# Kernel tuning notes

Hardware: AMD Instinct MI355X
Metric: run time of the kernel (lower is better)

The kernel has to match this reference:

```python
import jax, jax.numpy as jnp
import numpy as np

# dims
B, S, D, H, F = 4, 1024, 1024, 16, 4096
DH = D // H
THETA0 = 1.0   # base firing threshold of AdaptiveLIFNeuron
RHO = 0.9      # adaptation decay
EPS = 1e-5


def layer_norm(x, g, b):
    mu = jnp.mean(x, axis=-1, keepdims=True)
    var = jnp.mean((x - mu) ** 2, axis=-1, keepdims=True)
    return (x - mu) * jax.lax.rsqrt(var + EPS) * g + b


def spike(u):
    # Heaviside forward, sigmoid surrogate gradient (straight-through)
    sg = jax.nn.sigmoid(4.0 * u)
    hard = (u > 0).astype(u.dtype)
    return sg + jax.lax.stop_gradient(hard - sg)


def setup_inputs() -> dict:
    key = jax.random.key(0)
    ks = jax.random.split(key, 8)
    std = 0.02
    w = lambda k, shape: jax.random.normal(k, shape, jnp.float32) * std
    return {
        "x": jax.random.normal(ks[0], (B, S, D), jnp.float32),
        "Wq": w(ks[1], (D, D)), "bq": jnp.zeros((D,), jnp.float32),
        "Wk": w(ks[2], (D, D)), "bk": jnp.zeros((D,), jnp.float32),
        "Wv": w(ks[3], (D, D)), "bv": jnp.zeros((D,), jnp.float32),
        "Wo": w(ks[4], (D, D)), "bo": jnp.zeros((D,), jnp.float32),
        "g1": jnp.ones((D,), jnp.float32), "b1": jnp.zeros((D,), jnp.float32),
        "W1": w(ks[5], (D, F)), "bf1": jnp.zeros((F,), jnp.float32),
        "W2": w(ks[6], (F, D)), "bf2": jnp.zeros((D,), jnp.float32),
        "g2": jnp.ones((D,), jnp.float32), "b2": jnp.zeros((D,), jnp.float32),
        "decay": jnp.full((F,), 0.8, jnp.float32),  # per-feature membrane leak
        "beta": jnp.full((F,), 0.1, jnp.float32),   # per-feature threshold adaptation
    }


def reference(x, Wq, bq, Wk, bk, Wv, bv, Wo, bo, g1, b1, W1, bf1, W2, bf2, g2, b2, decay, beta):
    # --- causal multi-head self-attention (DSALayer) ---
    q = (x @ Wq + bq).reshape(B, S, H, DH)
    k = (x @ Wk + bk).reshape(B, S, H, DH)
    v = (x @ Wv + bv).reshape(B, S, H, DH)
    scores = jnp.einsum("bqhd,bkhd->bhqk", q, k) / np.sqrt(DH).astype(np.float32)
    causal = jnp.tril(jnp.ones((S, S), bool))
    scores = jnp.where(causal, scores, jnp.asarray(-1e9, scores.dtype))
    p = jax.nn.softmax(scores, axis=-1)
    attn = jnp.einsum("bhqk,bkhd->bqhd", p, v).reshape(B, S, D) @ Wo + bo
    h = layer_norm(x + attn, g1, b1)

    # --- feed-forward with per-timestep adaptive LIF recurrence ---
    ff = h @ W1 + bf1                      # [B, S, F]

    def step(carry, xt):
        vm, a = carry                      # membrane potential, adaptation
        vm = decay * vm + xt
        u = vm - (THETA0 + a)
        s = spike(u)
        vm = vm * (1.0 - s)                # hard reset on spike
        a = RHO * a + beta * s
        return (vm, a), s

    init = (jnp.zeros((B, F), x.dtype), jnp.zeros((B, F), x.dtype))
    _, spikes = jax.lax.scan(step, init, jnp.swapaxes(ff, 0, 1))  # scan over time
    spikes = jnp.swapaxes(spikes, 0, 1)    # [B, S, F]

    ff_out = spikes @ W2 + bf2
    return layer_norm(h + ff_out, g2, b2)
```

## Files before the change

### kernel.cpp

```cpp
#include <hip/hip_runtime.h>
#include <hip/hip_bf16.h>
#include <stdint.h>

#define Bsz 4
#define Ssz 1024
#define Dsz 1024
#define Hsz 16
#define Fsz 4096

typedef __hip_bfloat16 bf16;
typedef __attribute__((ext_vector_type(8))) short bf16x8;
typedef __attribute__((ext_vector_type(4))) float f32x4;

typedef __attribute__((address_space(1))) const void gvoid_t;
typedef __attribute__((address_space(3))) void svoid_t;

__device__ __forceinline__ void gload16(const bf16* g, bf16* l) {
    __builtin_amdgcn_global_load_lds((gvoid_t*)g, (svoid_t*)l, 16, 0, 0);
}

__global__ __launch_bounds__(256) void split_k(const float* __restrict__ src,
                                               bf16* __restrict__ hi,
                                               bf16* __restrict__ lo,
                                               const float* __restrict__ bq,
                                               const float* __restrict__ bk,
                                               const float* __restrict__ bv,
                                               float* __restrict__ bqkv) {
    const int i = (blockIdx.x * 256 + threadIdx.x) * 4;
    const float4 v = *(const float4*)(src + i);
    float vv[4] = {v.x, v.y, v.z, v.w};
    #pragma unroll
    for (int u = 0; u < 4; ++u) {
        const bf16 h = __float2bfloat16(vv[u]);
        hi[i + u] = h;
        lo[i + u] = __float2bfloat16(vv[u] - __bfloat162float(h));
    }
    if (blockIdx.x < 3) {
        const float* bsrc = (blockIdx.x == 0) ? bq : (blockIdx.x == 1) ? bk : bv;
        const int j = threadIdx.x * 4;
        *(float4*)(bqkv + blockIdx.x * 1024 + j) = *(const float4*)(bsrc + j);
    }
}

__global__ __launch_bounds__(256) void transpose_split4_k(const float* __restrict__ Wq,
                                                          const float* __restrict__ Wk,
                                                          const float* __restrict__ Wv,
                                                          const float* __restrict__ Wo,
                                                          bf16* __restrict__ qkv_hi,
                                                          bf16* __restrict__ qkv_lo,
                                                          bf16* __restrict__ wo_hi,
                                                          bf16* __restrict__ wo_lo) {
    __shared__ float tile[32][33];
    const int z = blockIdx.z;
    const float* in = (z == 0) ? Wq : (z == 1) ? Wk : (z == 2) ? Wv : Wo;
    const size_t WP = (size_t)Dsz * Dsz;
    bf16* hiT = (z < 3) ? qkv_hi + (size_t)z * WP : wo_hi;
    bf16* loT = (z < 3) ? qkv_lo + (size_t)z * WP : wo_lo;
    const int bx = blockIdx.x * 32, by = blockIdx.y * 32;
    const int tx = threadIdx.x, ty = threadIdx.y;
    #pragma unroll
    for (int i = 0; i < 32; i += 8)
        tile[ty + i][tx] = in[(size_t)(by + ty + i) * Dsz + bx + tx];
    __syncthreads();
    #pragma unroll
    for (int i = 0; i < 32; i += 8) {
        const float v = tile[tx][ty + i];
        const bf16 h = __float2bfloat16(v);
        const size_t o = (size_t)(bx + ty + i) * Dsz + by + tx;
        hiT[o] = h;
        loT[o] = __float2bfloat16(v - __bfloat162float(h));
    }
}

__global__ __launch_bounds__(256) void transpose_split_k(const float* __restrict__ in,
                                                         bf16* __restrict__ hiT,
                                                         bf16* __restrict__ loT,
                                                         int R, int C) {
    __shared__ float tile[32][33];
    const int bx = blockIdx.x * 32, by = blockIdx.y * 32;
    const int tx = threadIdx.x, ty = threadIdx.y;
    #pragma unroll
    for (int i = 0; i < 32; i += 8)
        tile[ty + i][tx] = in[(size_t)(by + ty + i) * C + bx + tx];
    __syncthreads();
    #pragma unroll
    for (int i = 0; i < 32; i += 8) {
        const float v = tile[tx][ty + i];
        const bf16 h = __float2bfloat16(v);
        const size_t o = (size_t)(bx + ty + i) * R + by + tx;
        hiT[o] = h;
        loT[o] = __float2bfloat16(v - __bfloat162float(h));
    }
}

__global__ __launch_bounds__(256) void transpose_cast_k(const float* __restrict__ in,
                                                        bf16* __restrict__ outT,
                                                        int R, int C) {
    __shared__ float tile[32][33];
    const int bx = blockIdx.x * 32, by = blockIdx.y * 32;
    const int tx = threadIdx.x, ty = threadIdx.y;
    #pragma unroll
    for (int i = 0; i < 32; i += 8)
        tile[ty + i][tx] = in[(size_t)(by + ty + i) * C + bx + tx];
    __syncthreads();
    #pragma unroll
    for (int i = 0; i < 32; i += 8)
        outT[(size_t)(bx + ty + i) * R + by + tx] = __float2bfloat16(tile[tx][ty + i]);
}

__global__ __launch_bounds__(256) void gemm3_bt(const bf16* __restrict__ Ah,
                                                const bf16* __restrict__ Al,
                                                const bf16* __restrict__ Bh,
                                                const bf16* __restrict__ Bl,
                                                const float* __restrict__ bias,
                                                float* __restrict__ Cf,
                                                int M, int N, int K) {
    __shared__ alignas(16) bf16 Ash[128 * 32];
    __shared__ alignas(16) bf16 Asl[128 * 32];
    __shared__ alignas(16) bf16 Bsh[128 * 32];
    __shared__ alignas(16) bf16 Bsl[128 * 32];
    const int t = threadIdx.x;
    const int lane = t & 63, wv = t >> 6;
    const int mw = wv >> 1, nw = wv & 1;
    const int m0 = blockIdx.y * 128, n0 = blockIdx.x * 128;
    const int z = blockIdx.z, nz = gridDim.z;
    const int Ks = K / nz, koff = z * Ks;
    const int r16 = lane & 15, q8 = (lane >> 4) * 8;
    const int arow = t >> 2, acol = (t & 3) * 8;

    const bf16* gAh = Ah + (size_t)(m0 + arow) * K + koff + acol;
    const bf16* gAl = Al + (size_t)(m0 + arow) * K + koff + acol;
    const bf16* gBh = Bh + (size_t)(n0 + arow) * K + koff + acol;
    const bf16* gBl = Bl + (size_t)(n0 + arow) * K + koff + acol;
    const size_t rK64 = (size_t)64 * K;
    bf16* lAh = Ash + wv * 512;
    bf16* lAl = Asl + wv * 512;
    bf16* lBh = Bsh + wv * 512;
    bf16* lBl = Bsl + wv * 512;

    f32x4 acc[4][4] = {};

    for (int k0 = 0; k0 < Ks; k0 += 32) {
        __syncthreads();
        gload16(gAh + k0, lAh);  gload16(gAh + k0 + rK64, lAh + 2048);
        gload16(gAl + k0, lAl);  gload16(gAl + k0 + rK64, lAl + 2048);
        gload16(gBh + k0, lBh);  gload16(gBh + k0 + rK64, lBh + 2048);
        gload16(gBl + k0, lBl);  gload16(gBl + k0 + rK64, lBl + 2048);
        __syncthreads();

        bf16x8 ah[4], al[4], bh[4], bl[4];
        #pragma unroll
        for (int rt = 0; rt < 4; ++rt) {
            const int ro = (64 * mw + 16 * rt + r16) * 32 + q8;
            ah[rt] = *(const bf16x8*)(Ash + ro);
            al[rt] = *(const bf16x8*)(Asl + ro);
        }
        #pragma unroll
        for (int ct = 0; ct < 4; ++ct) {
            const int co = (64 * nw + 16 * ct + r16) * 32 + q8;
            bh[ct] = *(const bf16x8*)(Bsh + co);
            bl[ct] = *(const bf16x8*)(Bsl + co);
        }
        #pragma unroll
        for (int rt = 0; rt < 4; ++rt)
            #pragma unroll
            for (int ct = 0; ct < 4; ++ct) {
                acc[rt][ct] = __builtin_amdgcn_mfma_f32_16x16x32_bf16(ah[rt], bh[ct], acc[rt][ct], 0, 0, 0);
                acc[rt][ct] = __builtin_amdgcn_mfma_f32_16x16x32_bf16(ah[rt], bl[ct], acc[rt][ct], 0, 0, 0);
                acc[rt][ct] = __builtin_amdgcn_mfma_f32_16x16x32_bf16(al[rt], bh[ct], acc[rt][ct], 0, 0, 0);
            }
    }

    float* Cz = Cf + (size_t)z * M * N;
    const int rowi = (lane >> 4) * 4;
    const int coli = lane & 15;
    #pragma unroll
    for (int ct = 0; ct < 4; ++ct) {
        const int col = n0 + 64 * nw + 16 * ct + coli;
        const float bv = (z == 0) ? bias[col] : 0.f;
        #pragma unroll
        for (int rt = 0; rt < 4; ++rt) {
            const int rowb = m0 + 64 * mw + 16 * rt + rowi;
            #pragma unroll
            for (int r = 0; r < 4; ++r)
                Cz[(size_t)(rowb + r) * N + col] = acc[rt][ct][r] + bv;
        }
    }
}

__global__ __launch_bounds__(256) void gemm3_qkv(const bf16* __restrict__ Ah,
                                                 const bf16* __restrict__ Al,
                                                 const bf16* __restrict__ Bh,
                                                 const bf16* __restrict__ Bl,
                                                 const float* __restrict__ bias,
                                                 bf16* __restrict__ qhi, bf16* __restrict__ qlo,
                                                 bf16* __restrict__ khi, bf16* __restrict__ klo,
                                                 bf16* __restrict__ vthi, bf16* __restrict__ vtlo) {
    const int K = Dsz;
    __shared__ alignas(16) bf16 Ash[128 * 32];
    __shared__ alignas(16) bf16 Asl[128 * 32];
    __shared__ alignas(16) bf16 Bsh[128 * 32];
    __shared__ alignas(16) bf16 Bsl[128 * 32];
    const int t = threadIdx.x;
    const int lane = t & 63, wv = t >> 6;
    const int mw = wv >> 1, nw = wv & 1;
    const int m0 = blockIdx.y * 128, n0 = blockIdx.x * 128;
    const int r16 = lane & 15, q8 = (lane >> 4) * 8;
    const int arow = t >> 2, acol = (t & 3) * 8;

    const bf16* gAh = Ah + (size_t)(m0 + arow) * K + acol;
    const bf16* gAl = Al + (size_t)(m0 + arow) * K + acol;
    const bf16* gBh = Bh + (size_t)(n0 + arow) * K + acol;
    const bf16* gBl = Bl + (size_t)(n0 + arow) * K + acol;
    const size_t rK64 = (size_t)64 * K;
    bf16* lAh = Ash + wv * 512;
    bf16* lAl = Asl + wv * 512;
    bf16* lBh = Bsh + wv * 512;
    bf16* lBl = Bsl + wv * 512;

    f32x4 acc[4][4] = {};

    for (int k0 = 0; k0 < K; k0 += 32) {
        __syncthreads();
        gload16(gAh + k0, lAh);  gload16(gAh + k0 + rK64, lAh + 2048);
        gload16(gAl + k0, lAl);  gload16(gAl + k0 + rK64, lAl + 2048);
        gload16(gBh + k0, lBh);  gload16(gBh + k0 + rK64, lBh + 2048);
        gload16(gBl + k0, lBl);  gload16(gBl + k0 + rK64, lBl + 2048);
        __syncthreads();

        bf16x8 ah[4], al[4], bh[4], bl[4];
        #pragma unroll
        for (int rt = 0; rt < 4; ++rt) {
            const int ro = (64 * mw + 16 * rt + r16) * 32 + q8;
            ah[rt] = *(const bf16x8*)(Ash + ro);
            al[rt] = *(const bf16x8*)(Asl + ro);
        }
        #pragma unroll
        for (int ct = 0; ct < 4; ++ct) {
            const int co = (64 * nw + 16 * ct + r16) * 32 + q8;
            bh[ct] = *(const bf16x8*)(Bsh + co);
            bl[ct] = *(const bf16x8*)(Bsl + co);
        }
        #pragma unroll
        for (int rt = 0; rt < 4; ++rt)
            #pragma unroll
            for (int ct = 0; ct < 4; ++ct) {
                acc[rt][ct] = __builtin_amdgcn_mfma_f32_16x16x32_bf16(ah[rt], bh[ct], acc[rt][ct], 0, 0, 0);
                acc[rt][ct] = __builtin_amdgcn_mfma_f32_16x16x32_bf16(ah[rt], bl[ct], acc[rt][ct], 0, 0, 0);
                acc[rt][ct] = __builtin_amdgcn_mfma_f32_16x16x32_bf16(al[rt], bh[ct], acc[rt][ct], 0, 0, 0);
            }
    }

    const int rowi = (lane >> 4) * 4;
    const int coli = lane & 15;
    if (n0 < 2048) {
        const float scale = (n0 < 1024) ? 0.125f : 1.0f;
        bf16* hip_ = (n0 < 1024) ? qhi : khi;
        bf16* lop_ = (n0 < 1024) ? qlo : klo;
        const int cbase = (n0 < 1024) ? n0 : (n0 - 1024);
        #pragma unroll
        for (int ct = 0; ct < 4; ++ct) {
            const int col = cbase + 64 * nw + 16 * ct + coli;
            const float bv = bias[n0 + 64 * nw + 16 * ct + coli];
            #pragma unroll
            for (int rt = 0; rt < 4; ++rt) {
                const int rowb = m0 + 64 * mw + 16 * rt + rowi;
                #pragma unroll
                for (int r = 0; r < 4; ++r) {
                    const float val = (acc[rt][ct][r] + bv) * scale;
                    const bf16 h = __float2bfloat16(val);
                    const size_t off = (size_t)(rowb + r) * Dsz + col;
                    hip_[off] = h;
                    lop_[off] = __float2bfloat16(val - __bfloat162float(h));
                }
            }
        }
    } else {
        #pragma unroll
        for (int ct = 0; ct < 4; ++ct) {
            const int col = n0 + 64 * nw + 16 * ct + coli;
            const float bv = bias[col];
            const int c2 = col - 2048;
            #pragma unroll
            for (int rt = 0; rt < 4; ++rt) {
                const int rowb = m0 + 64 * mw + 16 * rt + rowi;
                const int b = rowb >> 10, s = rowb & 1023;
                bf16 hv[4], lv[4];
                #pragma unroll
                for (int r = 0; r < 4; ++r) {
                    const float val = acc[rt][ct][r] + bv;
                    hv[r] = __float2bfloat16(val);
                    lv[r] = __float2bfloat16(val - __bfloat162float(hv[r]));
                }
                const size_t vo = (size_t)b * (16 * 64 * 1024) + (size_t)c2 * 1024 + s;
                *(uint2*)&vthi[vo] = *(const uint2*)hv;
                *(uint2*)&vtlo[vo] = *(const uint2*)lv;
            }
        }
    }
}

__global__ __launch_bounds__(256) void gemm1_bt(const bf16* __restrict__ A,
                                                const bf16* __restrict__ Bt,
                                                const float* __restrict__ bias,
                                                float* __restrict__ Cf,
                                                int M, int N, int K) {
    __shared__ alignas(16) bf16 As[128 * 32];
    __shared__ alignas(16) bf16 Bs[128 * 32];
    const int t = threadIdx.x;
    const int lane = t & 63, wv = t >> 6;
    const int mw = wv >> 1, nw = wv & 1;
    const int m0 = blockIdx.y * 128, n0 = blockIdx.x * 128;
    const int z = blockIdx.z, nz = gridDim.z;
    const int Ks = K / nz, koff = z * Ks;
    const int r16 = lane & 15, q8 = (lane >> 4) * 8;
    const int arow = t >> 2, acol = (t & 3) * 8;

    const bf16* gA = A + (size_t)(m0 + arow) * K + koff + acol;
    const bf16* gB = Bt + (size_t)(n0 + arow) * K + koff + acol;
    const size_t rK64 = (size_t)64 * K;
    bf16* lA = As + wv * 512;
    bf16* lB = Bs + wv * 512;

    f32x4 acc[4][4] = {};

    for (int k0 = 0; k0 < Ks; k0 += 32) {
        __syncthreads();
        gload16(gA + k0, lA);  gload16(gA + k0 + rK64, lA + 2048);
        gload16(gB + k0, lB);  gload16(gB + k0 + rK64, lB + 2048);
        __syncthreads();

        bf16x8 af[4], bf_[4];
        #pragma unroll
        for (int rt = 0; rt < 4; ++rt)
            af[rt] = *(const bf16x8*)(As + (64 * mw + 16 * rt + r16) * 32 + q8);
        #pragma unroll
        for (int ct = 0; ct < 4; ++ct)
            bf_[ct] = *(const bf16x8*)(Bs + (64 * nw + 16 * ct + r16) * 32 + q8);
        #pragma unroll
        for (int rt = 0; rt < 4; ++rt)
            #pragma unroll
            for (int ct = 0; ct < 4; ++ct)
                acc[rt][ct] = __builtin_amdgcn_mfma_f32_16x16x32_bf16(
                    af[rt], bf_[ct], acc[rt][ct], 0, 0, 0);
    }

    float* Cz = Cf + (size_t)z * M * N;
    const int rowi = (lane >> 4) * 4;
    const int coli = lane & 15;
    #pragma unroll
    for (int ct = 0; ct < 4; ++ct) {
        const int col = n0 + 64 * nw + 16 * ct + coli;
        const float bv = (z == 0) ? bias[col] : 0.f;
        #pragma unroll
        for (int rt = 0; rt < 4; ++rt) {
            const int rowb = m0 + 64 * mw + 16 * rt + rowi;
            #pragma unroll
            for (int r = 0; r < 4; ++r)
                Cz[(size_t)(rowb + r) * N + col] = acc[rt][ct][r] + bv;
        }
    }
}

__global__ __launch_bounds__(512) void attn_mfma_k(const bf16* __restrict__ qhp,
                                                   const bf16* __restrict__ qlp,
                                                   const bf16* __restrict__ khp,
                                                   const bf16* __restrict__ klp,
                                                   const bf16* __restrict__ vhp,
                                                   const bf16* __restrict__ vlp,
                                                   bf16* __restrict__ ohi,
                                                   bf16* __restrict__ olo) {
    __shared__ alignas(16) float Pf[256 * 68];

    const int bh = blockIdx.x;
    const int b = bh >> 4, h = bh & 15;
    const int pr = blockIdx.y;
    const int t = threadIdx.x, w = t >> 6, lane = t & 63;
    const int r16 = lane & 15, quad = lane >> 4;
    const int strip = (w < 4) ? pr : 7 - pr;
    const int qw = strip * 128 + 32 * (w & 3);

    bf16x8 aQh[2][2], aQl[2][2];
    #pragma unroll
    for (int mt = 0; mt < 2; ++mt) {
        const size_t qb = (size_t)(b * Ssz + qw + 16 * mt + r16) * Dsz + h * 64 + quad * 8;
        aQh[mt][0] = *(const bf16x8*)(qhp + qb);
        aQh[mt][1] = *(const bf16x8*)(qhp + qb + 32);
        aQl[mt][0] = *(const bf16x8*)(qlp + qb);
        aQl[mt][1] = *(const bf16x8*)(qlp + qb + 32);
    }

    f32x4 aco[2][4] = {};
    float lrun[2][4] = {};
    const int ntiles = (qw + 31) / 64 + 1;

    for (int kt = 0; kt < ntiles; ++kt) {
        #pragma unroll
        for (int nt = 0; nt < 4; ++nt) {
            const size_t kb = (size_t)(b * Ssz + kt * 64 + nt * 16 + r16) * Dsz + h * 64 + quad * 8;
            const bf16x8 bKh0 = *(const bf16x8*)(khp + kb);
            const bf16x8 bKh1 = *(const bf16x8*)(khp + kb + 32);
            const bf16x8 bKl0 = *(const bf16x8*)(klp + kb);
            const bf16x8 bKl1 = *(const bf16x8*)(klp + kb + 32);
            const int key = kt * 64 + nt * 16 + r16;
            #pragma unroll
            for (int mt = 0; mt < 2; ++mt) {
                f32x4 s = {};
                s = __builtin_amdgcn_mfma_f32_16x16x32_bf16(aQh[mt][0], bKh0, s, 0, 0, 0);
                s = __builtin_amdgcn_mfma_f32_16x16x32_bf16(aQh[mt][0], bKl0, s, 0, 0, 0);
                s = __builtin_amdgcn_mfma_f32_16x16x32_bf16(aQl[mt][0], bKh0, s, 0, 0, 0);
                s = __builtin_amdgcn_mfma_f32_16x16x32_bf16(aQh[mt][1], bKh1, s, 0, 0, 0);
                s = __builtin_amdgcn_mfma_f32_16x16x32_bf16(aQh[mt][1], bKl1, s, 0, 0, 0);
                s = __builtin_amdgcn_mfma_f32_16x16x32_bf16(aQl[mt][1], bKh1, s, 0, 0, 0);
                #pragma unroll
                for (int r = 0; r < 4; ++r) {
                    const int qrow = qw + 16 * mt + quad * 4 + r;
                    const float p = (key <= qrow) ? __expf(s[r]) : 0.f;
                    lrun[mt][r] += p;
                    Pf[(32 * w + 16 * mt + quad * 4 + r) * 68 + nt * 16 + r16] = p;
                }
            }
        }

        bf16x8 aPh[2][2], aPl[2][2];
        #pragma unroll
        for (int mt = 0; mt < 2; ++mt)
            #pragma unroll
            for (int ks = 0; ks < 2; ++ks) {
                const float* pr_ = &Pf[(32 * w + 16 * mt + r16) * 68 + ks * 32 + quad * 8];
                const float4 pa = *(const float4*)pr_;
                const float4 pb = *(const float4*)(pr_ + 4);
                const float pv[8] = {pa.x, pa.y, pa.z, pa.w, pb.x, pb.y, pb.z, pb.w};
                bf16 hv[8], lv[8];
                #pragma unroll
                for (int j = 0; j < 8; ++j) {
                    hv[j] = __float2bfloat16(pv[j]);
                    lv[j] = __float2bfloat16(pv[j] - __bfloat162float(hv[j]));
                }
                aPh[mt][ks] = *(const bf16x8*)hv;
                aPl[mt][ks] = *(const bf16x8*)lv;
            }

        #pragma unroll
        for (int nt = 0; nt < 4; ++nt) {
            const size_t vb = ((size_t)bh * 64 + nt * 16 + r16) * Ssz + kt * 64 + quad * 8;
            const bf16x8 bVh0 = *(const bf16x8*)(vhp + vb);
            const bf16x8 bVh1 = *(const bf16x8*)(vhp + vb + 32);
            const bf16x8 bVl0 = *(const bf16x8*)(vlp + vb);
            const bf16x8 bVl1 = *(const bf16x8*)(vlp + vb + 32);
            #pragma unroll
            for (int mt = 0; mt < 2; ++mt) {
                aco[mt][nt] = __builtin_amdgcn_mfma_f32_16x16x32_bf16(aPh[mt][0], bVh0, aco[mt][nt], 0, 0, 0);
                aco[mt][nt] = __builtin_amdgcn_mfma_f32_16x16x32_bf16(aPh[mt][0], bVl0, aco[mt][nt], 0, 0, 0);
                aco[mt][nt] = __builtin_amdgcn_mfma_f32_16x16x32_bf16(aPl[mt][0], bVh0, aco[mt][nt], 0, 0, 0);
                aco[mt][nt] = __builtin_amdgcn_mfma_f32_16x16x32_bf16(aPh[mt][1], bVh1, aco[mt][nt], 0, 0, 0);
                aco[mt][nt] = __builtin_amdgcn_mfma_f32_16x16x32_bf16(aPh[mt][1], bVl1, aco[mt][nt], 0, 0, 0);
                aco[mt][nt] = __builtin_amdgcn_mfma_f32_16x16x32_bf16(aPl[mt][1], bVh1, aco[mt][nt], 0, 0, 0);
            }
        }
    }

    #pragma unroll
    for (int mt = 0; mt < 2; ++mt)
        #pragma unroll
        for (int r = 0; r < 4; ++r) {
            float l = lrun[mt][r];
            l += __shfl_xor(l, 1); l += __shfl_xor(l, 2);
            l += __shfl_xor(l, 4); l += __shfl_xor(l, 8);
            lrun[mt][r] = l;
        }
    #pragma unroll
    for (int mt = 0; mt < 2; ++mt)
        #pragma unroll
        for (int nt = 0; nt < 4; ++nt)
            #pragma unroll
            for (int r = 0; r < 4; ++r) {
                const size_t off = (size_t)(b * Ssz + qw + 16 * mt + quad * 4 + r) * Dsz
                                   + h * 64 + nt * 16 + r16;
                const float val = aco[mt][nt][r] / lrun[mt][r];
                const bf16 hh = __float2bfloat16(val);
                ohi[off] = hh;
                olo[off] = __float2bfloat16(val - __bfloat162float(hh));
            }
}

__global__ __launch_bounds__(64) void scan_k(const float* __restrict__ ff,
                                             const float* __restrict__ decay,
                                             const float* __restrict__ beta,
                                             bf16* __restrict__ spikes) {
    const int idx = blockIdx.x * 64 + threadIdx.x;
    const int b = idx >> 12;
    const int f = idx & (Fsz - 1);
    const float dec = decay[f];
    const float bet = beta[f];
    const float* src = ff + (size_t)b * Ssz * Fsz + f;
    bf16* dst = spikes + (size_t)b * Ssz * Fsz + f;
    float vm = 0.f, a = 0.f;
    float buf[64];
    #pragma unroll
    for (int u = 0; u < 64; ++u) buf[u] = src[(size_t)u * Fsz];
    for (int gg = 0; gg < 16; ++gg) {
        #pragma unroll
        for (int sub = 0; sub < 4; ++sub) {
            const int g = gg * 4 + sub;
            #pragma unroll
            for (int u = 0; u < 16; ++u) {
                vm = dec * vm + buf[sub * 16 + u];
                const float uu = vm - (1.f + a);
                const float sp = (uu > 0.f) ? 1.f : 0.f;
                vm = (uu > 0.f) ? 0.f : vm;
                a = 0.9f * a + bet * sp;
                dst[(size_t)(g * 16 + u) * Fsz] = __float2bfloat16(sp);
            }
            if (g + 4 < 64) {
                #pragma unroll
                for (int u = 0; u < 16; ++u)
                    buf[sub * 16 + u] = src[(size_t)((g + 4) * 16 + u) * Fsz];
            }
        }
    }
}

__device__ __forceinline__ float block_sum(float val, float* ls, int t) {
    #pragma unroll
    for (int mm = 32; mm >= 1; mm >>= 1) val += __shfl_xor(val, mm);
    if ((t & 63) == 0) ls[t >> 6] = val;
    __syncthreads();
    const float r = ls[0] + ls[1] + ls[2] + ls[3];
    __syncthreads();
    return r;
}

__global__ __launch_bounds__(256) void ln1_k(const float* __restrict__ x,
                                             const float* __restrict__ ap0,
                                             const float* __restrict__ ap1,
                                             const float* __restrict__ g,
                                             const float* __restrict__ bb,
                                             bf16* __restrict__ h_hi,
                                             bf16* __restrict__ h_lo) {
    __shared__ float ls[4];
    const int row = blockIdx.x;
    const int t = threadIdx.x;
    const size_t base = (size_t)row * Dsz;
    float vv[4];
    #pragma unroll
    for (int i = 0; i < 4; ++i) {
        const int c = t + i * 256;
        vv[i] = x[base + c] + (ap0[base + c] + ap1[base + c]);
    }
    float s = vv[0] + vv[1] + vv[2] + vv[3];
    s = block_sum(s, ls, t);
    const float mu = s * (1.f / 1024.f);
    float qs = 0.f;
    #pragma unroll
    for (int i = 0; i < 4; ++i) { const float d = vv[i] - mu; qs += d * d; }
    qs = block_sum(qs, ls, t);
    const float rs = rsqrtf(qs * (1.f / 1024.f) + 1e-5f);
    #pragma unroll
    for (int i = 0; i < 4; ++i) {
        const int c = t + i * 256;
        const float o = (vv[i] - mu) * rs * g[c] + bb[c];
        const bf16 hi = __float2bfloat16(o);
        h_hi[base + c] = hi;
        h_lo[base + c] = __float2bfloat16(o - __bfloat162float(hi));
    }
}

__global__ __launch_bounds__(256) void ln2_k(const bf16* __restrict__ h_hi,
                                             const bf16* __restrict__ h_lo,
                                             const float* __restrict__ fo0,
                                             const float* __restrict__ fo1,
                                             const float* __restrict__ g,
                                             const float* __restrict__ bb,
                                             float* __restrict__ out) {
    __shared__ float ls[4];
    const int row = blockIdx.x;
    const int t = threadIdx.x;
    const size_t base = (size_t)row * Dsz;
    float vv[4];
    #pragma unroll
    for (int i = 0; i < 4; ++i) {
        const int c = t + i * 256;
        const float h = __bfloat162float(h_hi[base + c]) + __bfloat162float(h_lo[base + c]);
        vv[i] = h + (fo0[base + c] + fo1[base + c]);
    }
    float s = vv[0] + vv[1] + vv[2] + vv[3];
    s = block_sum(s, ls, t);
    const float mu = s * (1.f / 1024.f);
    float qs = 0.f;
    #pragma unroll
    for (int i = 0; i < 4; ++i) { const float d = vv[i] - mu; qs += d * d; }
    qs = block_sum(qs, ls, t);
    const float rs = rsqrtf(qs * (1.f / 1024.f) + 1e-5f);
    #pragma unroll
    for (int i = 0; i < 4; ++i) {
        const int c = t + i * 256;
        out[base + c] = (vv[i] - mu) * rs * g[c] + bb[c];
    }
}

extern "C" void kernel_launch(void* const* d_in, const int* in_sizes, int n_in,
                              void* d_out, int out_size, void* d_ws, size_t ws_size,
                              hipStream_t stream) {
    const float* x    = (const float*)d_in[0];
    const float* Wq   = (const float*)d_in[1];
    const float* bq   = (const float*)d_in[2];
    const float* Wk   = (const float*)d_in[3];
    const float* bk   = (const float*)d_in[4];
    const float* Wv   = (const float*)d_in[5];
    const float* bv   = (const float*)d_in[6];
    const float* Wo   = (const float*)d_in[7];
    const float* bo   = (const float*)d_in[8];
    const float* g1   = (const float*)d_in[9];
    const float* b1   = (const float*)d_in[10];
    const float* W1   = (const float*)d_in[11];
    const float* bf1  = (const float*)d_in[12];
    const float* W2   = (const float*)d_in[13];
    const float* bf2  = (const float*)d_in[14];
    const float* g2   = (const float*)d_in[15];
    const float* b2   = (const float*)d_in[16];
    const float* dec  = (const float*)d_in[17];
    const float* beta = (const float*)d_in[18];

    const size_t BSD = (size_t)Bsz * Ssz * Dsz;
    const size_t BSF = (size_t)Bsz * Ssz * Fsz;

    char* ws = (char*)d_ws;
    char* A3 = ws;
    char* A1 = A3 + BSF * 4;
    char* A2 = A1 + BSF * 2;
    char* A4 = A2 + (size_t)Dsz * Fsz * 2 * 2;
    float* bqkv = (float*)(A4 + BSD * 4);

    bf16* qhi   = (bf16*)(A3);
    bf16* qlo   = (bf16*)(A3 + BSD * 2);
    bf16* khi   = (bf16*)(A3 + BSD * 4);
    bf16* klo   = (bf16*)(A3 + BSD * 6);
    float* attnp = (float*)(A3);
    float* ffb   = (float*)(A3);
    float* ffout = (float*)(A3);

    bf16* xhi    = (bf16*)(A1);
    bf16* xlo    = (bf16*)(A1 + BSD * 2);
    bf16* athi   = (bf16*)(A1);
    bf16* atlo   = (bf16*)(A1 + BSD * 2);
    bf16* spikes = (bf16*)(A1);

    const size_t WP = (size_t)Dsz * Dsz;
    bf16* Wqkv_hi = (bf16*)(A2);
    bf16* Wqkv_lo = (bf16*)(A2 + WP * 3 * 2);
    bf16* WoThi   = (bf16*)(A2 + WP * 6 * 2);
    bf16* WoTlo   = (bf16*)(A2 + WP * 7 * 2);
    bf16* W1Thi   = (bf16*)(A2);
    bf16* W1Tlo   = (bf16*)(A2 + (size_t)Dsz * Fsz * 2);
    bf16* W2T     = (bf16*)(A2);

    bf16* vthi  = (bf16*)(A4);
    bf16* vtlo  = (bf16*)(A4 + BSD * 2);
    bf16* h_hi  = (bf16*)(A4);
    bf16* h_lo  = (bf16*)(A4 + BSD * 2);

    (void)ws_size; (void)in_sizes; (void)n_in; (void)out_size;

    const dim3 tb(32, 8);
    const int MBS = Bsz * Ssz;

    split_k<<<BSD / 1024, 256, 0, stream>>>(x, xhi, xlo, bq, bk, bv, bqkv);
    transpose_split4_k<<<dim3(32, 32, 4), tb, 0, stream>>>(
        Wq, Wk, Wv, Wo, Wqkv_hi, Wqkv_lo, WoThi, WoTlo);

    gemm3_qkv<<<dim3(3072 / 128, MBS / 128), 256, 0, stream>>>(
        xhi, xlo, Wqkv_hi, Wqkv_lo, bqkv, qhi, qlo, khi, klo, vthi, vtlo);

    attn_mfma_k<<<dim3(Bsz * Hsz, 4), 512, 0, stream>>>(
        qhi, qlo, khi, klo, vthi, vtlo, athi, atlo);

    gemm3_bt<<<dim3(Dsz / 128, MBS / 128, 2), 256, 0, stream>>>(
        athi, atlo, WoThi, WoTlo, bo, attnp, MBS, Dsz, Dsz);
    ln1_k<<<MBS, 256, 0, stream>>>(x, attnp, attnp + (size_t)MBS * Dsz,
                                   g1, b1, h_hi, h_lo);

    transpose_split_k<<<dim3(Fsz / 32, Dsz / 32), tb, 0, stream>>>(W1, W1Thi, W1Tlo, Dsz, Fsz);
    gemm3_bt<<<dim3(Fsz / 128, MBS / 128, 1), 256, 0, stream>>>(
        h_hi, h_lo, W1Thi, W1Tlo, bf1, ffb, MBS, Fsz, Dsz);

    scan_k<<<Bsz * Fsz / 64, 64, 0, stream>>>(ffb, dec, beta, spikes);

    transpose_cast_k<<<dim3(Dsz / 32, Fsz / 32), tb, 0, stream>>>(W2, W2T, Fsz, Dsz);
    gemm1_bt<<<dim3(Dsz / 128, MBS / 128, 2), 256, 0, stream>>>(
        spikes, W2T, bf2, ffout, MBS, Dsz, Fsz);

    ln2_k<<<MBS, 256, 0, stream>>>(h_hi, h_lo, ffout, ffout + (size_t)MBS * Dsz,
                                   g2, b2, (float*)d_out);
}
```

Measured before the change: 591.8 us.

## Remap GEMM tiles for XCD-local L2 reuse and merge prep kernels

GEMM kernels now use a 1D grid whose block index is remapped so that consecutive blocks, which land on different XCDs round-robin, get column tiles grouped per XCD. Each XCD's L2 then sees a contiguous band of B columns, which should improve cache reuse of weight tiles. The x split and the four-weight transpose/split are also merged into one prep kernel, saving a launch. The remap assumes the N tile count is divisible by 8 and relies on the hardware's round-robin block dispatch across XCDs.

Measured after the change: 585.3 us. About the same (-1.1%).

```diff
diff --git a/kernel.cpp b/kernel.cpp
--- a/kernel.cpp
+++ b/kernel.cpp
@@ -19,56 +19,68 @@
     __builtin_amdgcn_global_load_lds((gvoid_t*)g, (svoid_t*)l, 16, 0, 0);
 }
 
-__global__ __launch_bounds__(256) void split_k(const float* __restrict__ src,
-                                               bf16* __restrict__ hi,
-                                               bf16* __restrict__ lo,
-                                               const float* __restrict__ bq,
-                                               const float* __restrict__ bk,
-                                               const float* __restrict__ bv,
-                                               float* __restrict__ bqkv) {
-    const int i = (blockIdx.x * 256 + threadIdx.x) * 4;
-    const float4 v = *(const float4*)(src + i);
-    float vv[4] = {v.x, v.y, v.z, v.w};
-    #pragma unroll
-    for (int u = 0; u < 4; ++u) {
-        const bf16 h = __float2bfloat16(vv[u]);
-        hi[i + u] = h;
-        lo[i + u] = __float2bfloat16(vv[u] - __bfloat162float(h));
-    }
-    if (blockIdx.x < 3) {
-        const float* bsrc = (blockIdx.x == 0) ? bq : (blockIdx.x == 1) ? bk : bv;
-        const int j = threadIdx.x * 4;
-        *(float4*)(bqkv + blockIdx.x * 1024 + j) = *(const float4*)(bsrc + j);
-    }
-}
-
-__global__ __launch_bounds__(256) void transpose_split4_k(const float* __restrict__ Wq,
-                                                          const float* __restrict__ Wk,
-                                                          const float* __restrict__ Wv,
-                                                          const float* __restrict__ Wo,
-                                                          bf16* __restrict__ qkv_hi,
-                                                          bf16* __restrict__ qkv_lo,
-                                                          bf16* __restrict__ wo_hi,
-                                                          bf16* __restrict__ wo_lo) {
-    __shared__ float tile[32][33];
-    const int z = blockIdx.z;
-    const float* in = (z == 0) ? Wq : (z == 1) ? Wk : (z == 2) ? Wv : Wo;
-    const size_t WP = (size_t)Dsz * Dsz;
-    bf16* hiT = (z < 3) ? qkv_hi + (size_t)z * WP : wo_hi;
-    bf16* loT = (z < 3) ? qkv_lo + (size_t)z * WP : wo_lo;
-    const int bx = blockIdx.x * 32, by = blockIdx.y * 32;
-    const int tx = threadIdx.x, ty = threadIdx.y;
-    #pragma unroll
-    for (int i = 0; i < 32; i += 8)
-        tile[ty + i][tx] = in[(size_t)(by + ty + i) * Dsz + bx + tx];
-    __syncthreads();
-    #pragma unroll
-    for (int i = 0; i < 32; i += 8) {
-        const float v = tile[tx][ty + i];
-        const bf16 h = __float2bfloat16(v);
-        const size_t o = (size_t)(bx + ty + i) * Dsz + by + tx;
-        hiT[o] = h;
-        loT[o] = __float2bfloat16(v - __bfloat162float(h));
+__device__ __forceinline__ void xcd_tiles(int p, int nT, int& n0, int& m0) {
+    const int W8 = nT >> 3;
+    const int n = (p & 7) * W8 + ((p >> 3) % W8);
+    const int m = p / (8 * W8);
+    n0 = n << 7;
+    m0 = m << 7;
+}
+
+__global__ __launch_bounds__(256) void prep_k(const float* __restrict__ x,
+                                              const float* __restrict__ Wq,
+                                              const float* __restrict__ Wk,
+                                              const float* __restrict__ Wv,
+                                              const float* __restrict__ Wo,
+                                              bf16* __restrict__ xhi,
+                                              bf16* __restrict__ xlo,
+                                              bf16* __restrict__ qkv_hi,
+                                              bf16* __restrict__ qkv_lo,
+                                              bf16* __restrict__ wo_hi,
+                                              bf16* __restrict__ wo_lo,
+                                              const float* __restrict__ bq,
+                                              const float* __restrict__ bk,
+                                              const float* __restrict__ bv,
+                                              float* __restrict__ bqkv) {
+    const int id = blockIdx.x;
+    const int t = threadIdx.x;
+    if (id < 4096) {
+        __shared__ float tile[32][33];
+        const int z = id >> 10, rem = id & 1023;
+        const int bx = (rem & 31) * 32, by = (rem >> 5) * 32;
+        const float* in = (z == 0) ? Wq : (z == 1) ? Wk : (z == 2) ? Wv : Wo;
+        const size_t WP = (size_t)Dsz * Dsz;
+        bf16* hiT = (z < 3) ? qkv_hi + (size_t)z * WP : wo_hi;
+        bf16* loT = (z < 3) ? qkv_lo + (size_t)z * WP : wo_lo;
+        const int tx = t & 31, ty = t >> 5;
+        #pragma unroll
+        for (int i = 0; i < 32; i += 8)
+            tile[ty + i][tx] = in[(size_t)(by + ty + i) * Dsz + bx + tx];
+        __syncthreads();
+        #pragma unroll
+        for (int i = 0; i < 32; i += 8) {
+            const float v = tile[tx][ty + i];
+            const bf16 h = __float2bfloat16(v);
+            const size_t o = (size_t)(bx + ty + i) * Dsz + by + tx;
+            hiT[o] = h;
+            loT[o] = __float2bfloat16(v - __bfloat162float(h));
+        }
+    } else {
+        const int sb = id - 4096;
+        const int i = (sb * 256 + t) * 4;
+        const float4 v = *(const float4*)(x + i);
+        float vv[4] = {v.x, v.y, v.z, v.w};
+        #pragma unroll
+        for (int u = 0; u < 4; ++u) {
+            const bf16 h = __float2bfloat16(vv[u]);
+            xhi[i + u] = h;
+            xlo[i + u] = __float2bfloat16(vv[u] - __bfloat162float(h));
+        }
+        if (sb < 3) {
+            const float* bsrc = (sb == 0) ? bq : (sb == 1) ? bk : bv;
+            const int j = t * 4;
+            *(float4*)(bqkv + sb * 1024 + j) = *(const float4*)(bsrc + j);
+        }
     }
 }
 
@@ -122,7 +134,8 @@
     const int t = threadIdx.x;
     const int lane = t & 63, wv = t >> 6;
     const int mw = wv >> 1, nw = wv & 1;
-    const int m0 = blockIdx.y * 128, n0 = blockIdx.x * 128;
+    int n0, m0;
+    xcd_tiles(blockIdx.x, N >> 7, n0, m0);
     const int z = blockIdx.z, nz = gridDim.z;
     const int Ks = K / nz, koff = z * Ks;
     const int r16 = lane & 15, q8 = (lane >> 4) * 8;
@@ -204,7 +217,8 @@
     const int t = threadIdx.x;
     const int lane = t & 63, wv = t >> 6;
     const int mw = wv >> 1, nw = wv & 1;
-    const int m0 = blockIdx.y * 128, n0 = blockIdx.x * 128;
+    int n0, m0;
+    xcd_tiles(blockIdx.x, 3072 >> 7, n0, m0);
     const int r16 = lane & 15, q8 = (lane >> 4) * 8;
     const int arow = t >> 2, acol = (t & 3) * 8;
 
@@ -310,7 +324,8 @@
     const int t = threadIdx.x;
     const int lane = t & 63, wv = t >> 6;
     const int mw = wv >> 1, nw = wv & 1;
-    const int m0 = blockIdx.y * 128, n0 = blockIdx.x * 128;
+    int n0, m0;
+    xcd_tiles(blockIdx.x, N >> 7, n0, m0);
     const int z = blockIdx.z, nz = gridDim.z;
     const int Ks = K / nz, koff = z * Ks;
     const int r16 = lane & 15, q8 = (lane >> 4) * 8;
@@ -665,29 +680,29 @@
     const dim3 tb(32, 8);
     const int MBS = Bsz * Ssz;
 
-    split_k<<<BSD / 1024, 256, 0, stream>>>(x, xhi, xlo, bq, bk, bv, bqkv);
-    transpose_split4_k<<<dim3(32, 32, 4), tb, 0, stream>>>(
-        Wq, Wk, Wv, Wo, Wqkv_hi, Wqkv_lo, WoThi, WoTlo);
-
-    gemm3_qkv<<<dim3(3072 / 128, MBS / 128), 256, 0, stream>>>(
+    prep_k<<<8192, 256, 0, stream>>>(x, Wq, Wk, Wv, Wo, xhi, xlo,
+                                     Wqkv_hi, Wqkv_lo, WoThi, WoTlo,
+                                     bq, bk, bv, bqkv);
+
+    gemm3_qkv<<<dim3(24 * 32), 256, 0, stream>>>(
         xhi, xlo, Wqkv_hi, Wqkv_lo, bqkv, qhi, qlo, khi, klo, vthi, vtlo);
 
     attn_mfma_k<<<dim3(Bsz * Hsz, 4), 512, 0, stream>>>(
         qhi, qlo, khi, klo, vthi, vtlo, athi, atlo);
 
-    gemm3_bt<<<dim3(Dsz / 128, MBS / 128, 2), 256, 0, stream>>>(
+    gemm3_bt<<<dim3(8 * 32, 1, 2), 256, 0, stream>>>(
         athi, atlo, WoThi, WoTlo, bo, attnp, MBS, Dsz, Dsz);
     ln1_k<<<MBS, 256, 0, stream>>>(x, attnp, attnp + (size_t)MBS * Dsz,
                                    g1, b1, h_hi, h_lo);
 
     transpose_split_k<<<dim3(Fsz / 32, Dsz / 32), tb, 0, stream>>>(W1, W1Thi, W1Tlo, Dsz, Fsz);
-    gemm3_bt<<<dim3(Fsz / 128, MBS / 128, 1), 256, 0, stream>>>(
+    gemm3_bt<<<dim3(32 * 32, 1, 1), 256, 0, stream>>>(
         h_hi, h_lo, W1Thi, W1Tlo, bf1, ffb, MBS, Fsz, Dsz);
 
     scan_k<<<Bsz * Fsz / 64, 64, 0, stream>>>(ffb, dec, beta, spikes);
 
     transpose_cast_k<<<dim3(Dsz / 32, Fsz / 32), tb, 0, stream>>>(W2, W2T, Fsz, Dsz);
-    gemm1_bt<<<dim3(Dsz / 128, MBS / 128, 2), 256, 0, stream>>>(
+    gemm1_bt<<<dim3(8 * 32, 1, 2), 256, 0, stream>>>(
         spikes, W2T, bf2, ffout, MBS, Dsz, Fsz);
 
     ln2_k<<<MBS, 256, 0, stream>>>(h_hi, h_lo, ffout, ffout + (size_t)MBS * Dsz,
```
